# Kernel optimization log

Measured on AMD Instinct MI355X. Metric: run time of the kernel, lower is better.

## Reference

```python
import jax, jax.numpy as jnp
import numpy as np

NB = 50  # nb_steps
IN_D = 64
HID = 128
B = 256


def _cc_weights(nb):
    # Faithful port of UMNN compute_cc_weights (Clenshaw-Curtis quadrature)
    lam = np.arange(0, nb + 1).reshape(-1, 1).astype(np.float64)
    lam = np.cos((lam @ lam.T) * np.pi / nb)
    lam[:, 0] = 0.5
    lam[:, -1] = 0.5 * lam[:, -1]
    lam = lam * 2.0 / nb
    W = np.arange(0, nb + 1).reshape(-1, 1).astype(np.float64)
    W[np.arange(1, nb + 1, 2)] = 0
    W = 2.0 / (1.0 - W ** 2)
    W[0] = 1
    W[np.arange(1, nb + 1, 2)] = 0
    cc = (lam.T @ W)[:, 0].astype(np.float32)              # [nb+1]
    steps = np.cos(np.arange(0, nb + 1) * np.pi / nb).astype(np.float32)  # [nb+1]
    return jnp.asarray(cc), jnp.asarray(steps)


def setup_inputs() -> dict:
    key = jax.random.key(0)
    ks = jax.random.split(key, 16)
    d = {}
    d["x"] = jax.random.normal(ks[0], (B, 1), dtype=jnp.float32)
    d["h"] = jax.random.normal(ks[1], (B, IN_D - 1), dtype=jnp.float32)

    def lin(kw, kb, fan_in, fan_out):
        s = 1.0 / np.sqrt(fan_in)
        w = jax.random.uniform(kw, (fan_in, fan_out), jnp.float32, -s, s)
        b = jax.random.uniform(kb, (fan_out,), jnp.float32, -s, s)
        return w, b

    # Integrand MLP: in_d -> 128 -> 128 -> 1
    d["iw0"], d["ib0"] = lin(ks[2], ks[3], IN_D, HID)
    d["iw1"], d["ib1"] = lin(ks[4], ks[5], HID, HID)
    d["iw2"], d["ib2"] = lin(ks[6], ks[7], HID, 1)
    # Outer net: (in_d-1) -> 128 -> 128 -> 2
    d["nw0"], d["nb0"] = lin(ks[8], ks[9], IN_D - 1, HID)
    d["nw1"], d["nb1"] = lin(ks[10], ks[11], HID, HID)
    d["nw2"], d["nb2"] = lin(ks[12], ks[13], HID, 2)
    return d


def reference(x, h, iw0, ib0, iw1, ib1, iw2, ib2, nw0, nb0, nw1, nb1, nw2, nb2):
    cc, steps = _cc_weights(NB)  # [S1], [S1]
    S1 = NB + 1
    b = x.shape[0]

    # ----- outer quadrature: integral over t in [0, x] -----
    # t[b, i] = 0 + (x - 0) * (steps[i] + 1) / 2
    t = x[:, None, :] * (steps[None, :, None] + 1.0) / 2.0          # [B, S1, 1]

    # ----- inner UMNN: integral over s in [t, xmax], xmax = max(t) + 10 -----
    xmax = jnp.max(t) + 10.0
    s = t[:, :, None, :] + (xmax - t)[:, :, None, :] * (steps[None, None, :, None] + 1.0) / 2.0  # [B,S1,S1,1]

    hb = jnp.broadcast_to(h[:, None, None, :], (b, S1, S1, h.shape[1]))
    inp = jnp.concatenate([s, hb], axis=-1)                         # [B,S1,S1,in_d]

    # PostiveIntegrandNN: Lin-ReLU-Lin-ReLU-Lin-ELU, then + 1.0
    a = jax.nn.relu(inp @ iw0 + ib0)
    a = jax.nn.relu(a @ iw1 + ib1)
    f = jax.nn.elu(a @ iw2 + ib2) + 1.0                              # [B,S1,S1,1]

    # inner Clenshaw-Curtis reduction: z * (xT - x0) / 2
    inner = jnp.sum(f * cc[None, None, :, None], axis=2) * (xmax - t) / 2.0   # [B,S1,1]

    # outer reduction: integral from 0 to x
    outer = jnp.sum(inner * cc[None, :, None], axis=1) * x / 2.0    # [B,1]

    # outer dense net on h -> offset / scaling
    o = jax.nn.relu(h @ nw0 + nb0)
    o = jax.nn.relu(o @ nw1 + nb1)
    o = o @ nw2 + nb2                                               # [B,2]
    offset = o[:, 0:1]
    scaling = jnp.exp(o[:, 1:2])
    return scaling * outer + offset
```

## Files before the change

### kernel.cpp

```cpp
#include <hip/hip_runtime.h>
#include <math.h>

#define NBQ 50
#define S1 51
#define NPTS 2601
#define NTILES 163
#define IN_D 64
#define HID 128
#define BSZ 256
#define NCHUNK 8
#define NUMAX 21

typedef __bf16 bf16x8 __attribute__((ext_vector_type(8)));
typedef float  f32x4  __attribute__((ext_vector_type(4)));

#define WS_CC     0
#define WS_STEPS  64
#define WS_XMAX   128
#define WS_BASE   256
#define WS_SCAL   33024
#define WS_OFF    33280
#define WS_PART   33536
#define WS_W1BF   41728

__global__ void k_prep(const float* __restrict__ x, const float* __restrict__ h,
                       const float* __restrict__ iw0, const float* __restrict__ ib0,
                       const float* __restrict__ iw1,
                       const float* __restrict__ nw0, const float* __restrict__ nb0,
                       const float* __restrict__ nw1, const float* __restrict__ nb1,
                       const float* __restrict__ nw2, const float* __restrict__ nb2,
                       float* __restrict__ ws) {
    int blk = blockIdx.x;
    int tid = threadIdx.x;

    if (blk < 64) {
        int idx  = blk * 256 + tid;
        int e    = idx & 7;
        int lane = (idx >> 3) & 63;
        int fk   = idx >> 9;
        int kk   = fk & 3;
        int nt   = fk >> 2;
        int k = kk * 32 + (lane >> 4) * 8 + e;
        int n = nt * 16 + (lane & 15);
        __bf16* w1bf = (__bf16*)(ws + WS_W1BF);
        w1bf[idx] = (__bf16)iw1[k * HID + n];
        return;
    }

    __shared__ float s_steps[S1];
    __shared__ float s_red[4];
    __shared__ float s_h[IN_D - 1];
    __shared__ float s_o0[HID];
    __shared__ float s_part[4];

    if (blk == 64) {
        int t = tid;
        if (t < S1) {
            double st = cos((double)t * M_PI / (double)NBQ);
            s_steps[t] = (float)st;
            ws[WS_STEPS + t] = (float)st;
            double acc = 0.0;
            for (int i = 0; i <= NBQ; ++i) {
                double Wi;
                if (i == 0)       Wi = 1.0;
                else if (i & 1)   Wi = 0.0;
                else              Wi = 2.0 / (1.0 - (double)i * (double)i);
                double lam;
                if (t == 0)  lam = 0.5;
                else         lam = cos((double)i * (double)t * M_PI / (double)NBQ);
                if (t == NBQ) lam *= 0.5;
                lam *= 2.0 / (double)NBQ;
                acc += lam * Wi;
            }
            ws[WS_CC + t] = (float)acc;
        }
        __syncthreads();
        float xb = x[t];
        float m = -1e30f;
        for (int i = 0; i < S1; ++i)
            m = fmaxf(m, xb * (s_steps[i] + 1.0f) * 0.5f);
        for (int off = 32; off > 0; off >>= 1)
            m = fmaxf(m, __shfl_down(m, off));
        if ((t & 63) == 0) s_red[t >> 6] = m;
        __syncthreads();
        if (t == 0) {
            float mm = fmaxf(fmaxf(s_red[0], s_red[1]), fmaxf(s_red[2], s_red[3]));
            ws[WS_XMAX] = mm + 10.0f;
        }
        return;
    }

    int b = blk - 65;
    int n = tid;
    bool act = (n < HID);
    if (act && n < IN_D - 1) s_h[n] = h[b * (IN_D - 1) + n];
    __syncthreads();
    float o1 = 0.0f;
    if (act) {
        float accB = ib0[n];
        float acc0 = nb0[n];
        for (int d = 0; d < IN_D - 1; ++d) {
            float hv = s_h[d];
            accB = fmaf(hv, iw0[(1 + d) * HID + n], accB);
            acc0 = fmaf(hv, nw0[d * HID + n], acc0);
        }
        ws[WS_BASE + b * HID + n] = accB;
        s_o0[n] = fmaxf(acc0, 0.0f);
    }
    __syncthreads();
    if (act) {
        float acc1 = nb1[n];
        for (int m = 0; m < HID; ++m)
            acc1 = fmaf(s_o0[m], nw1[m * HID + n], acc1);
        o1 = fmaxf(acc1, 0.0f);
    }
    float p0 = act ? o1 * nw2[n * 2 + 0] : 0.0f;
    float p1 = act ? o1 * nw2[n * 2 + 1] : 0.0f;
    for (int off = 32; off > 0; off >>= 1) {
        p0 += __shfl_down(p0, off);
        p1 += __shfl_down(p1, off);
    }
    int lane = tid & 63, w = tid >> 6;
    if (lane == 0 && w < 2) { s_part[w * 2] = p0; s_part[w * 2 + 1] = p1; }
    __syncthreads();
    if (tid == 0) {
        ws[WS_OFF + b]  = s_part[0] + s_part[2] + nb2[0];
        ws[WS_SCAL + b] = expf(s_part[1] + s_part[3] + nb2[1]);
    }
}

__global__ __launch_bounds__(256, 3) void k3_mfma(
        const float* __restrict__ x,
        const float* __restrict__ iw0,
        const float* __restrict__ ib1,
        const float* __restrict__ iw2,
        const float* __restrict__ ib2,
        float* __restrict__ ws) {
    __shared__ float s_cc[S1];
    __shared__ float s_ti[S1];
    __shared__ float s_w[S1];
    __shared__ float s_sjh[S1];
    __shared__ float s_ccw[S1];
    __shared__ bf16x8 bfr_lds[2][4][4][64];
    __shared__ float zlds[4][NUMAX][17];

    int blk  = blockIdx.x;
    int b    = blk >> 3;
    int c    = blk & 7;
    int tid  = threadIdx.x;
    int wave = tid >> 6;
    int lane = tid & 63;
    int col  = lane & 15;
    int g    = lane >> 4;

    float xmax = ws[WS_XMAX];
    float xb   = x[b];
    float b2   = ib2[0];

    if (tid < S1) {
        float st = ws[WS_STEPS + tid];
        float cc = ws[WS_CC + tid];
        float ti = xb * (st + 1.0f) * 0.5f;
        float w  = xmax - ti;
        s_cc[tid]  = cc;
        s_ti[tid]  = ti;
        s_w[tid]   = w;
        s_sjh[tid] = (st + 1.0f) * 0.5f;
        s_ccw[tid] = cc * w;
    }

    const bf16x8* w1f = (const bf16x8*)(ws + WS_W1BF);
    bf16x8 Af[2][4];
#pragma unroll
    for (int nt = 0; nt < 2; ++nt) {
        int NT = wave * 2 + nt;
#pragma unroll
        for (int kk = 0; kk < 4; ++kk)
            Af[nt][kk] = w1f[(NT * 4 + kk) * 64 + lane];
    }

    const float* basep = ws + WS_BASE + b * HID;
    int m0 = wave * 32 + g * 8;
    f32x4 w0a = *(const f32x4*)(iw0 + m0);
    f32x4 w0b = *(const f32x4*)(iw0 + m0 + 4);
    f32x4 bsa = *(const f32x4*)(basep + m0);
    f32x4 bsb = *(const f32x4*)(basep + m0 + 4);

    f32x4 accInit[2], iw2v[2];
#pragma unroll
    for (int nt = 0; nt < 2; ++nt) {
        int n0 = (wave * 2 + nt) * 16 + g * 4;
        accInit[nt] = *(const f32x4*)(ib1 + n0);
        iw2v[nt]    = *(const f32x4*)(iw2 + n0);
    }

    int NU = (c <= 2) ? 21 : 20;
    int G  = (NU + 3) >> 2;

    __syncthreads();

#pragma unroll
    for (int t = 0; t < 4; ++t) {
        int u = t;
        if (u < NU) {
            int p  = (c + 8 * u) * 16 + col;
            int pc = (p < NPTS) ? p : (NPTS - 1);
            int i  = (int)(((unsigned)pc * 10281u) >> 19);
            int j  = pc - i * 51;
            float s = fmaf(s_w[i], s_sjh[j], s_ti[i]);
            bf16x8 bfr;
#pragma unroll
            for (int e = 0; e < 4; ++e) {
                bfr[e]     = (__bf16)fmaxf(fmaf(s, w0a[e], bsa[e]), 0.0f);
                bfr[4 + e] = (__bf16)fmaxf(fmaf(s, w0b[e], bsb[e]), 0.0f);
            }
            bfr_lds[0][t][wave][lane] = bfr;
        }
    }
    __syncthreads();

    for (int grp = 0; grp < G; ++grp) {
        int nb = grp + 1;
        if (nb < G) {
            int ubase = nb * 4;
#pragma unroll
            for (int t = 0; t < 4; ++t) {
                int u = ubase + t;
                if (u < NU) {
                    int p  = (c + 8 * u) * 16 + col;
                    int pc = (p < NPTS) ? p : (NPTS - 1);
                    int i  = (int)(((unsigned)pc * 10281u) >> 19);
                    int j  = pc - i * 51;
                    float s = fmaf(s_w[i], s_sjh[j], s_ti[i]);
                    bf16x8 bfr;
#pragma unroll
                    for (int e = 0; e < 4; ++e) {
                        bfr[e]     = (__bf16)fmaxf(fmaf(s, w0a[e], bsa[e]), 0.0f);
                        bfr[4 + e] = (__bf16)fmaxf(fmaf(s, w0b[e], bsb[e]), 0.0f);
                    }
                    bfr_lds[nb & 1][t][wave][lane] = bfr;
                }
            }
        }

        int buf = grp & 1;
        int ubase = grp * 4;
#pragma unroll
        for (int t = 0; t < 4; ++t) {
            int u = ubase + t;
            if (u < NU) {
                bf16x8 f0 = bfr_lds[buf][t][0][lane];
                bf16x8 f1 = bfr_lds[buf][t][1][lane];
                bf16x8 f2 = bfr_lds[buf][t][2][lane];
                bf16x8 f3 = bfr_lds[buf][t][3][lane];
                f32x4 a0 = __builtin_amdgcn_mfma_f32_16x16x32_bf16(Af[0][0], f0, accInit[0], 0, 0, 0);
                f32x4 a1 = __builtin_amdgcn_mfma_f32_16x16x32_bf16(Af[1][0], f0, accInit[1], 0, 0, 0);
                a0 = __builtin_amdgcn_mfma_f32_16x16x32_bf16(Af[0][1], f1, a0, 0, 0, 0);
                a1 = __builtin_amdgcn_mfma_f32_16x16x32_bf16(Af[1][1], f1, a1, 0, 0, 0);
                a0 = __builtin_amdgcn_mfma_f32_16x16x32_bf16(Af[0][2], f2, a0, 0, 0, 0);
                a1 = __builtin_amdgcn_mfma_f32_16x16x32_bf16(Af[1][2], f2, a1, 0, 0, 0);
                a0 = __builtin_amdgcn_mfma_f32_16x16x32_bf16(Af[0][3], f3, a0, 0, 0, 0);
                a1 = __builtin_amdgcn_mfma_f32_16x16x32_bf16(Af[1][3], f3, a1, 0, 0, 0);

                float za = 0.f, zb = 0.f;
#pragma unroll
                for (int q = 0; q < 4; ++q) {
                    za = fmaf(fmaxf(a0[q], 0.0f), iw2v[0][q], za);
                    zb = fmaf(fmaxf(a1[q], 0.0f), iw2v[1][q], zb);
                }
                float z = za + zb;
                z += __shfl_xor(z, 16);
                z += __shfl_xor(z, 32);
                if (lane < 16) zlds[wave][u][lane] = z;
            }
        }
        __syncthreads();
    }

    float vsum = 0.0f;
    int npass = (NU + 15) >> 4;
    for (int pass = 0; pass < npass; ++pass) {
        int u = pass * 16 + wave * 4 + g;
        if (u < NU) {
            int p = (c + 8 * u) * 16 + col;
            if (p < NPTS) {
                float z = zlds[0][u][col] + zlds[1][u][col]
                        + zlds[2][u][col] + zlds[3][u][col] + b2;
                float f = (z > 0.0f) ? (z + 1.0f) : __expf(z);
                int i = (int)(((unsigned)p * 10281u) >> 19);
                int j = p - i * 51;
                vsum += s_ccw[i] * s_cc[j] * f;
            }
        }
    }
#pragma unroll
    for (int off = 1; off < 64; off <<= 1)
        vsum += __shfl_xor(vsum, off);
    if (lane == 0)
        ws[WS_PART + blk * 4 + wave] = vsum * 0.5f;
}

__global__ void k4_final(const float* __restrict__ x, const float* __restrict__ ws,
                         float* __restrict__ out) {
    int b = threadIdx.x;
    float sum = 0.0f;
#pragma unroll
    for (int c = 0; c < 32; ++c) sum += ws[WS_PART + b * 32 + c];
    out[b] = ws[WS_SCAL + b] * sum * x[b] * 0.5f + ws[WS_OFF + b];
}

extern "C" void kernel_launch(void* const* d_in, const int* in_sizes, int n_in,
                              void* d_out, int out_size, void* d_ws, size_t ws_size,
                              hipStream_t stream) {
    const float* x   = (const float*)d_in[0];
    const float* h   = (const float*)d_in[1];
    const float* iw0 = (const float*)d_in[2];
    const float* ib0 = (const float*)d_in[3];
    const float* iw1 = (const float*)d_in[4];
    const float* ib1 = (const float*)d_in[5];
    const float* iw2 = (const float*)d_in[6];
    const float* ib2 = (const float*)d_in[7];
    const float* nw0 = (const float*)d_in[8];
    const float* nb0 = (const float*)d_in[9];
    const float* nw1 = (const float*)d_in[10];
    const float* nb1 = (const float*)d_in[11];
    const float* nw2 = (const float*)d_in[12];
    const float* nb2 = (const float*)d_in[13];
    float* ws  = (float*)d_ws;
    float* out = (float*)d_out;

    hipLaunchKernelGGL(k_prep, dim3(64 + 1 + BSZ), dim3(256), 0, stream,
                       x, h, iw0, ib0, iw1, nw0, nb0, nw1, nb1, nw2, nb2, ws);
    hipLaunchKernelGGL(k3_mfma, dim3(BSZ * NCHUNK), dim3(256), 0, stream,
                       x, iw0, ib1, iw2, ib2, ws);
    hipLaunchKernelGGL(k4_final, dim3(1), dim3(BSZ), 0, stream, x, ws, out);
}
```

Baseline: 50.42 us.

## Halve block count per batch, precompute per-point tables, single-buffer feature LDS

Each batch row is now split into 4 chunks instead of 8, so each block handles roughly twice as many 16-point tiles and block count drops from 2048 to 1024. Per-point s values and quadrature weights are precomputed into LDS tables at block start, replacing the per-row arrays and index math in the main loop. The double-buffered prefetch of first-layer activations is replaced by a single buffer with an extra barrier per group, and launch bounds are raised to 4 blocks per SM. Together these aim to amortise per-block setup and raise occupancy, but they lose the overlap between feature generation and MFMA work and leave fewer blocks to fill the GPU.

```diff
diff --git a/kernel.cpp b/kernel.cpp
--- a/kernel.cpp
+++ b/kernel.cpp
@@ -8,8 +8,8 @@
 #define IN_D 64
 #define HID 128
 #define BSZ 256
-#define NCHUNK 8
-#define NUMAX 21
+#define NCHUNK 4
+#define NUMAX 41
 
 typedef __bf16 bf16x8 __attribute__((ext_vector_type(8)));
 typedef float  f32x4  __attribute__((ext_vector_type(4)));
@@ -129,24 +129,21 @@
     }
 }
 
-__global__ __launch_bounds__(256, 3) void k3_mfma(
+__global__ __launch_bounds__(256, 4) void k3_mfma(
         const float* __restrict__ x,
         const float* __restrict__ iw0,
         const float* __restrict__ ib1,
         const float* __restrict__ iw2,
         const float* __restrict__ ib2,
         float* __restrict__ ws) {
-    __shared__ float s_cc[S1];
-    __shared__ float s_ti[S1];
-    __shared__ float s_w[S1];
-    __shared__ float s_sjh[S1];
-    __shared__ float s_ccw[S1];
-    __shared__ bf16x8 bfr_lds[2][4][4][64];
+    __shared__ bf16x8 bfr_lds[4][4][64];
     __shared__ float zlds[4][NUMAX][17];
+    __shared__ float s_tbl[NUMAX][16];
+    __shared__ float w_tbl[NUMAX][16];
 
     int blk  = blockIdx.x;
-    int b    = blk >> 3;
-    int c    = blk & 7;
+    int b    = blk >> 2;
+    int c    = blk & 3;
     int tid  = threadIdx.x;
     int wave = tid >> 6;
     int lane = tid & 63;
@@ -157,16 +154,22 @@
     float xb   = x[b];
     float b2   = ib2[0];
 
-    if (tid < S1) {
-        float st = ws[WS_STEPS + tid];
-        float cc = ws[WS_CC + tid];
-        float ti = xb * (st + 1.0f) * 0.5f;
-        float w  = xmax - ti;
-        s_cc[tid]  = cc;
-        s_ti[tid]  = ti;
-        s_w[tid]   = w;
-        s_sjh[tid] = (st + 1.0f) * 0.5f;
-        s_ccw[tid] = cc * w;
+    int NU = (c < 3) ? 41 : 40;
+    int G  = (NU + 3) >> 2;
+
+    for (int e = tid; e < NU * 16; e += 256) {
+        int u  = e >> 4;
+        int cl = e & 15;
+        int p  = (c + 4 * u) * 16 + cl;
+        int pc = (p < NPTS) ? p : (NPTS - 1);
+        int i  = (int)(((unsigned)pc * 10281u) >> 19);
+        int j  = pc - i * 51;
+        float sti = ws[WS_STEPS + i];
+        float stj = ws[WS_STEPS + j];
+        float ti  = xb * (sti + 1.0f) * 0.5f;
+        float w   = xmax - ti;
+        s_tbl[u][cl] = fmaf(w, (stj + 1.0f) * 0.5f, ti);
+        w_tbl[u][cl] = ws[WS_CC + i] * ws[WS_CC + j] * w;
     }
 
     const bf16x8* w1f = (const bf16x8*)(ws + WS_W1BF);
@@ -194,65 +197,33 @@
         iw2v[nt]    = *(const f32x4*)(iw2 + n0);
     }
 
-    int NU = (c <= 2) ? 21 : 20;
-    int G  = (NU + 3) >> 2;
-
     __syncthreads();
 
-#pragma unroll
-    for (int t = 0; t < 4; ++t) {
-        int u = t;
-        if (u < NU) {
-            int p  = (c + 8 * u) * 16 + col;
-            int pc = (p < NPTS) ? p : (NPTS - 1);
-            int i  = (int)(((unsigned)pc * 10281u) >> 19);
-            int j  = pc - i * 51;
-            float s = fmaf(s_w[i], s_sjh[j], s_ti[i]);
-            bf16x8 bfr;
-#pragma unroll
-            for (int e = 0; e < 4; ++e) {
-                bfr[e]     = (__bf16)fmaxf(fmaf(s, w0a[e], bsa[e]), 0.0f);
-                bfr[4 + e] = (__bf16)fmaxf(fmaf(s, w0b[e], bsb[e]), 0.0f);
-            }
-            bfr_lds[0][t][wave][lane] = bfr;
-        }
-    }
-    __syncthreads();
-
     for (int grp = 0; grp < G; ++grp) {
-        int nb = grp + 1;
-        if (nb < G) {
-            int ubase = nb * 4;
-#pragma unroll
-            for (int t = 0; t < 4; ++t) {
-                int u = ubase + t;
-                if (u < NU) {
-                    int p  = (c + 8 * u) * 16 + col;
-                    int pc = (p < NPTS) ? p : (NPTS - 1);
-                    int i  = (int)(((unsigned)pc * 10281u) >> 19);
-                    int j  = pc - i * 51;
-                    float s = fmaf(s_w[i], s_sjh[j], s_ti[i]);
-                    bf16x8 bfr;
-#pragma unroll
-                    for (int e = 0; e < 4; ++e) {
-                        bfr[e]     = (__bf16)fmaxf(fmaf(s, w0a[e], bsa[e]), 0.0f);
-                        bfr[4 + e] = (__bf16)fmaxf(fmaf(s, w0b[e], bsb[e]), 0.0f);
-                    }
-                    bfr_lds[nb & 1][t][wave][lane] = bfr;
-                }
-            }
-        }
-
-        int buf = grp & 1;
         int ubase = grp * 4;
 #pragma unroll
         for (int t = 0; t < 4; ++t) {
             int u = ubase + t;
             if (u < NU) {
-                bf16x8 f0 = bfr_lds[buf][t][0][lane];
-                bf16x8 f1 = bfr_lds[buf][t][1][lane];
-                bf16x8 f2 = bfr_lds[buf][t][2][lane];
-                bf16x8 f3 = bfr_lds[buf][t][3][lane];
+                float s = s_tbl[u][col];
+                bf16x8 bfr;
+#pragma unroll
+                for (int e = 0; e < 4; ++e) {
+                    bfr[e]     = (__bf16)fmaxf(fmaf(s, w0a[e], bsa[e]), 0.0f);
+                    bfr[4 + e] = (__bf16)fmaxf(fmaf(s, w0b[e], bsb[e]), 0.0f);
+                }
+                bfr_lds[t][wave][lane] = bfr;
+            }
+        }
+        __syncthreads();
+#pragma unroll
+        for (int t = 0; t < 4; ++t) {
+            int u = ubase + t;
+            if (u < NU) {
+                bf16x8 f0 = bfr_lds[t][0][lane];
+                bf16x8 f1 = bfr_lds[t][1][lane];
+                bf16x8 f2 = bfr_lds[t][2][lane];
+                bf16x8 f3 = bfr_lds[t][3][lane];
                 f32x4 a0 = __builtin_amdgcn_mfma_f32_16x16x32_bf16(Af[0][0], f0, accInit[0], 0, 0, 0);
                 f32x4 a1 = __builtin_amdgcn_mfma_f32_16x16x32_bf16(Af[1][0], f0, accInit[1], 0, 0, 0);
                 a0 = __builtin_amdgcn_mfma_f32_16x16x32_bf16(Af[0][1], f1, a0, 0, 0, 0);
@@ -282,14 +253,12 @@
     for (int pass = 0; pass < npass; ++pass) {
         int u = pass * 16 + wave * 4 + g;
         if (u < NU) {
-            int p = (c + 8 * u) * 16 + col;
+            int p = (c + 4 * u) * 16 + col;
             if (p < NPTS) {
                 float z = zlds[0][u][col] + zlds[1][u][col]
                         + zlds[2][u][col] + zlds[3][u][col] + b2;
                 float f = (z > 0.0f) ? (z + 1.0f) : __expf(z);
-                int i = (int)(((unsigned)p * 10281u) >> 19);
-                int j = p - i * 51;
-                vsum += s_ccw[i] * s_cc[j] * f;
+                vsum += w_tbl[u][col] * f;
             }
         }
     }
@@ -305,7 +274,7 @@
     int b = threadIdx.x;
     float sum = 0.0f;
 #pragma unroll
-    for (int c = 0; c < 32; ++c) sum += ws[WS_PART + b * 32 + c];
+    for (int c = 0; c < 16; ++c) sum += ws[WS_PART + b * 16 + c];
     out[b] = ws[WS_SCAL + b] * sum * x[b] * 0.5f + ws[WS_OFF + b];
 }
 
```

After: 49.84 us. About the same (-1.1%).
